# Kernel tuning notes

Measured on AMD Instinct MI355X. Metric: run time of the kernel, lower is better.

The kernel has to match this reference:

```python
import jax, jax.numpy as jnp
import numpy as np

IN_UNITS = 128
N_DRUG, N_DIS, N_EDGE = 10000, 5000, 2000000


def setup_inputs() -> dict:
    key = jax.random.key(0)
    ks = jax.random.split(key, 10)
    s1 = 1.0 / np.sqrt(2 * IN_UNITS)
    s2 = 1.0 / np.sqrt(128)
    s3 = 1.0 / np.sqrt(64)
    return {
        "drug_feat": jax.random.normal(ks[0], (N_DRUG, IN_UNITS), dtype=jnp.float32),
        "dis_feat": jax.random.normal(ks[1], (N_DIS, IN_UNITS), dtype=jnp.float32),
        "edge_index": jax.random.randint(ks[2], (2, N_EDGE), 0, N_DIS, dtype=jnp.int64),
        "W1": jax.random.uniform(ks[3], (128, 2 * IN_UNITS), jnp.float32, -s1, s1),
        "b1": jax.random.uniform(ks[4], (128,), jnp.float32, -s1, s1),
        "W2": jax.random.uniform(ks[5], (64, 128), jnp.float32, -s2, s2),
        "b2": jax.random.uniform(ks[6], (64,), jnp.float32, -s2, s2),
        "W3": jax.random.uniform(ks[7], (1, 64), jnp.float32, -s3, s3),
        "b3": jax.random.uniform(ks[8], (1,), jnp.float32, -s3, s3),
    }


def reference(drug_feat, dis_feat, edge_index, W1, b1, W2, b2, W3, b3):
    # Gather endpoint features and concat along feature dim: [E, 2*in_units]
    edge_feat = jnp.concatenate(
        (drug_feat[edge_index[0]], dis_feat[edge_index[1]]), axis=1
    )
    # 3-layer MLP (Dropout is identity in eval mode)
    h = jax.nn.relu(edge_feat @ W1.T + b1)  # [E, 128]
    h = jax.nn.relu(h @ W2.T + b2)          # [E, 64]
    return h @ W3.T + b3                     # [E, 1]
```

## Files before the change

kernel.cpp:

```cpp
#include <hip/hip_runtime.h>


typedef __bf16 bf16x8 __attribute__((ext_vector_type(8)));
typedef unsigned short u16x8 __attribute__((ext_vector_type(8)));
typedef float f32x4 __attribute__((ext_vector_type(4)));

static __device__ __forceinline__ unsigned short f2b(float f) {
  unsigned int u = __builtin_bit_cast(unsigned int, f);
  u += 0x7FFFu + ((u >> 16) & 1u);
  return (unsigned short)(u >> 16);
}

static __device__ __forceinline__ f32x4 mfma_bf16(u16x8 a, u16x8 b, f32x4 c) {
  return __builtin_amdgcn_mfma_f32_16x16x32_bf16(
      __builtin_bit_cast(bf16x8, a), __builtin_bit_cast(bf16x8, b), c, 0, 0, 0);
}

__global__ void cvt_tables(const float* __restrict__ a, const float* __restrict__ b,
                           unsigned short* __restrict__ oa, unsigned short* __restrict__ ob,
                           int na, int nb) {
  const int t = blockIdx.x * blockDim.x + threadIdx.x;
  const int ta = na >> 3;
  const float* src;
  unsigned short* dst;
  int i;
  if (t < ta) {
    src = a; dst = oa; i = t;
  } else {
    i = t - ta;
    if (i >= (nb >> 3)) return;
    src = b; dst = ob;
  }
  const float4 f0 = *(const float4*)(src + i * 8);
  const float4 f1 = *(const float4*)(src + i * 8 + 4);
  u16x8 v;
  v[0] = f2b(f0.x); v[1] = f2b(f0.y); v[2] = f2b(f0.z); v[3] = f2b(f0.w);
  v[4] = f2b(f1.x); v[5] = f2b(f1.y); v[6] = f2b(f1.z); v[7] = f2b(f1.w);
  *(u16x8*)(dst + i * 8) = v;
}

__global__ void cvt_weights(const float* __restrict__ W1, const float* __restrict__ W2,
                            unsigned short* __restrict__ o1, unsigned short* __restrict__ o2) {
  const int t = blockIdx.x * blockDim.x + threadIdx.x;
  if (t < 4096) {
    const int l = t & 63, kt = (t >> 6) & 7, nt = t >> 9;
    const int n = 16 * nt + (l & 15), k0 = 32 * kt + 8 * (l >> 4);
    const float* src = W1 + n * 256 + k0;
    u16x8 v;
#pragma unroll
    for (int j = 0; j < 8; ++j) v[j] = f2b(src[j]);
    *(u16x8*)(o1 + t * 8) = v;
  } else if (t < 5120) {
    const int u = t - 4096;
    const int l = u & 63, kt = (u >> 6) & 3, nt = u >> 8;
    const int n = 16 * nt + (l & 15), k0 = 32 * kt + 8 * (l >> 4);
    const float* src = W2 + n * 128 + k0;
    u16x8 v;
#pragma unroll
    for (int j = 0; j < 8; ++j) v[j] = f2b(src[j]);
    *(u16x8*)(o2 + u * 8) = v;
  }
}

__global__ __launch_bounds__(512, 4) void mlp_fused(
    const unsigned short* __restrict__ drugB, const unsigned short* __restrict__ disB,
    const int* __restrict__ eidx, const unsigned short* __restrict__ w1frag,
    const unsigned short* __restrict__ w2frag, const float* __restrict__ b1,
    const float* __restrict__ b2, const float* __restrict__ W3,
    const float* __restrict__ b3, float* __restrict__ out, int E) {
  __shared__ __align__(16) unsigned char smem[65536 + 2048];
  unsigned char* Abase = smem;
  float* partials = (float*)(smem + 65536);

  const int tid = threadIdx.x;
  const int w = tid >> 6;
  const int wm = w >> 2;
  const int wn = w & 3;
  const int l = tid & 63;
  const int l15 = l & 15;
  const int lq = l >> 4;
  const int e0 = blockIdx.x * 128;

  {
    const int r = tid >> 2;
    const int q = tid & 3;
    int e = e0 + r;
    if (e >= E) e = E - 1;
    const int idx = (q < 2) ? eidx[e] : eidx[E + e];
    const unsigned short* src = ((q < 2) ? drugB : disB) + (long)idx * 128 + (q & 1) * 64;
    unsigned char* rowp = Abase + r * 512;
    const int base = q * 128;
    const int swz = (r & 7) << 4;
#pragma unroll
    for (int c = 0; c < 8; ++c) {
      const u16x8 v = *(const u16x8*)(src + c * 8);
      *(u16x8*)(rowp + ((base + c * 16) ^ swz)) = v;
    }
  }

  u16x8 w2f[4];
#pragma unroll
  for (int kt = 0; kt < 4; ++kt)
    w2f[kt] = *(const u16x8*)(w2frag + ((wn * 4 + kt) * 64 + l) * 8);
  const float b1v0 = b1[32 * wn + l15];
  const float b1v1 = b1[32 * wn + 16 + l15];
  const float b2v = b2[16 * wn + l15];
  const float w3v = W3[16 * wn + l15];
  __syncthreads();

  f32x4 acc1[4][2];
#pragma unroll
  for (int mti = 0; mti < 4; ++mti) {
    acc1[mti][0] = (f32x4){0.f, 0.f, 0.f, 0.f};
    acc1[mti][1] = (f32x4){0.f, 0.f, 0.f, 0.f};
  }
  const unsigned short* w1p = w1frag + ((2 * wn) * 8 * 64 + l) * 8;
  u16x8 nf0 = *(const u16x8*)(w1p);
  u16x8 nf1 = *(const u16x8*)(w1p + 512 * 8);
#pragma unroll
  for (int kt = 0; kt < 8; ++kt) {
    const u16x8 c0 = nf0, c1 = nf1;
    if (kt < 7) {
      nf0 = *(const u16x8*)(w1p + (kt + 1) * 64 * 8);
      nf1 = *(const u16x8*)(w1p + (512 + (kt + 1) * 64) * 8);
    }
#pragma unroll
    for (int mti = 0; mti < 4; ++mti) {
      const int row = 16 * (4 * wm + mti) + l15;
      const u16x8 a = *(const u16x8*)(Abase + row * 512 + ((64 * kt + 16 * lq) ^ ((row & 7) << 4)));
      acc1[mti][0] = mfma_bf16(a, c0, acc1[mti][0]);
      acc1[mti][1] = mfma_bf16(a, c1, acc1[mti][1]);
    }
  }
  __syncthreads();

#pragma unroll
  for (int mti = 0; mti < 4; ++mti) {
#pragma unroll
    for (int ntl = 0; ntl < 2; ++ntl) {
      const int col = 32 * wn + 16 * ntl + l15;
      const float bv = ntl ? b1v1 : b1v0;
#pragma unroll
      for (int i = 0; i < 4; ++i) {
        const int row = 16 * (4 * wm + mti) + 4 * lq + i;
        float h = acc1[mti][ntl][i] + bv;
        h = h > 0.f ? h : 0.f;
        *(unsigned short*)(Abase + row * 256 + (((unsigned)col * 2) ^ ((row & 7) << 4))) = f2b(h);
      }
    }
  }
  __syncthreads();

  f32x4 acc2[4];
#pragma unroll
  for (int mti = 0; mti < 4; ++mti) acc2[mti] = (f32x4){0.f, 0.f, 0.f, 0.f};
#pragma unroll
  for (int kt = 0; kt < 4; ++kt) {
#pragma unroll
    for (int mti = 0; mti < 4; ++mti) {
      const int row = 16 * (4 * wm + mti) + l15;
      const u16x8 a = *(const u16x8*)(Abase + row * 256 + ((64 * kt + 16 * lq) ^ ((row & 7) << 4)));
      acc2[mti] = mfma_bf16(a, w2f[kt], acc2[mti]);
    }
  }

  float p[16];
#pragma unroll
  for (int mti = 0; mti < 4; ++mti)
#pragma unroll
    for (int i = 0; i < 4; ++i) {
      float h = acc2[mti][i] + b2v;
      h = h > 0.f ? h : 0.f;
      p[mti * 4 + i] = h * w3v;
    }
  float a8[8];
#pragma unroll
  for (int j = 0; j < 8; ++j) {
    const bool hi = (l15 & 1);
    const float give = hi ? p[2 * j] : p[2 * j + 1];
    const float keep = hi ? p[2 * j + 1] : p[2 * j];
    a8[j] = keep + __shfl_xor(give, 1, 64);
  }
  float a4[4];
#pragma unroll
  for (int j = 0; j < 4; ++j) {
    const bool hi = (l15 & 2);
    const float give = hi ? a8[2 * j] : a8[2 * j + 1];
    const float keep = hi ? a8[2 * j + 1] : a8[2 * j];
    a4[j] = keep + __shfl_xor(give, 2, 64);
  }
  float a2[2];
#pragma unroll
  for (int j = 0; j < 2; ++j) {
    const bool hi = (l15 & 4);
    const float give = hi ? a4[2 * j] : a4[2 * j + 1];
    const float keep = hi ? a4[2 * j + 1] : a4[2 * j];
    a2[j] = keep + __shfl_xor(give, 4, 64);
  }
  float d;
  {
    const bool hi = (l15 & 8);
    const float give = hi ? a2[0] : a2[1];
    const float keep = hi ? a2[1] : a2[0];
    d = keep + __shfl_xor(give, 8, 64);
  }
  const int row = 16 * (4 * wm + (l15 >> 2)) + 4 * lq + (l15 & 3);
  partials[wn * 128 + row] = d;
  __syncthreads();

  if (tid < 128) {
    const int e = e0 + tid;
    if (e < E) {
      out[e] = partials[tid] + partials[128 + tid] + partials[256 + tid] +
               partials[384 + tid] + b3[0];
    }
  }
}

extern "C" void kernel_launch(void* const* d_in, const int* in_sizes, int n_in,
                              void* d_out, int out_size, void* d_ws, size_t ws_size,
                              hipStream_t stream) {
  const float* drug = (const float*)d_in[0];
  const float* dis = (const float*)d_in[1];
  const int* eidx = (const int*)d_in[2];
  const float* W1 = (const float*)d_in[3];
  const float* b1 = (const float*)d_in[4];
  const float* W2 = (const float*)d_in[5];
  const float* b2 = (const float*)d_in[6];
  const float* W3 = (const float*)d_in[7];
  const float* b3 = (const float*)d_in[8];
  float* out = (float*)d_out;

  const int na = in_sizes[0];
  const int nb = in_sizes[1];
  const int E = in_sizes[2] / 2;

  unsigned short* ws = (unsigned short*)d_ws;
  unsigned short* drugB = ws;
  unsigned short* disB = ws + na;
  unsigned short* w1f = ws + na + nb;
  unsigned short* w2f = w1f + 128 * 256;

  const int tct = (na + nb) >> 3;
  cvt_tables<<<(tct + 255) / 256, 256, 0, stream>>>(drug, dis, drugB, disB, na, nb);
  cvt_weights<<<20, 256, 0, stream>>>(W1, W2, w1f, w2f);

  const int grid = (E + 127) / 128;
  mlp_fused<<<grid, 512, 0, stream>>>(drugB, disB, eidx, w1f, w2f, b1, b2, W3, b3, out, E);
}
```

Before: 273.8 us.

## Transpose MFMA operands so weights are A and edges are B, halve block size

Blocks now handle 64 edges with 256 threads (4 waves), and each wave owns a slice of output features across all 64 edges. The MFMA operands are swapped so weight fragments form the A operand and gathered edge rows form the B operand. This lets bias, ReLU and the W3 dot product run per lane over 4 consecutive features, replacing the long shuffle-reduction tree with two cross-lane xor shuffles, and lets layer-1 activations be stored as 8-byte ushort4 writes. Smaller blocks with half the shared memory should allow more resident blocks per CU, but each wave now reads more LDS A-tiles per weight fragment and there are twice as many blocks.

New measurement: 245.2 us. 10.4% less time.

```diff
diff --git a/kernel.cpp b/kernel.cpp
--- a/kernel.cpp
+++ b/kernel.cpp
@@ -43,8 +43,8 @@
                             unsigned short* __restrict__ o1, unsigned short* __restrict__ o2) {
   const int t = blockIdx.x * blockDim.x + threadIdx.x;
   if (t < 4096) {
-    const int l = t & 63, kt = (t >> 6) & 7, nt = t >> 9;
-    const int n = 16 * nt + (l & 15), k0 = 32 * kt + 8 * (l >> 4);
+    const int l = t & 63, kt = (t >> 6) & 7, ut = t >> 9;
+    const int n = 16 * ut + (l & 15), k0 = 32 * kt + 8 * (l >> 4);
     const float* src = W1 + n * 256 + k0;
     u16x8 v;
 #pragma unroll
@@ -62,24 +62,22 @@
   }
 }
 
-__global__ __launch_bounds__(512, 4) void mlp_fused(
+__global__ __launch_bounds__(256, 4) void mlp_fused(
     const unsigned short* __restrict__ drugB, const unsigned short* __restrict__ disB,
     const int* __restrict__ eidx, const unsigned short* __restrict__ w1frag,
     const unsigned short* __restrict__ w2frag, const float* __restrict__ b1,
     const float* __restrict__ b2, const float* __restrict__ W3,
     const float* __restrict__ b3, float* __restrict__ out, int E) {
-  __shared__ __align__(16) unsigned char smem[65536 + 2048];
+  __shared__ __align__(16) unsigned char smem[32768 + 1024];
   unsigned char* Abase = smem;
-  float* partials = (float*)(smem + 65536);
+  float* partials = (float*)(smem + 32768);
 
   const int tid = threadIdx.x;
-  const int w = tid >> 6;
-  const int wm = w >> 2;
-  const int wn = w & 3;
+  const int wn = tid >> 6;
   const int l = tid & 63;
   const int l15 = l & 15;
   const int lq = l >> 4;
-  const int e0 = blockIdx.x * 128;
+  const int e0 = blockIdx.x * 64;
 
   {
     const int r = tid >> 2;
@@ -102,19 +100,19 @@
 #pragma unroll
   for (int kt = 0; kt < 4; ++kt)
     w2f[kt] = *(const u16x8*)(w2frag + ((wn * 4 + kt) * 64 + l) * 8);
-  const float b1v0 = b1[32 * wn + l15];
-  const float b1v1 = b1[32 * wn + 16 + l15];
-  const float b2v = b2[16 * wn + l15];
-  const float w3v = W3[16 * wn + l15];
-  __syncthreads();
-
-  f32x4 acc1[4][2];
-#pragma unroll
-  for (int mti = 0; mti < 4; ++mti) {
-    acc1[mti][0] = (f32x4){0.f, 0.f, 0.f, 0.f};
-    acc1[mti][1] = (f32x4){0.f, 0.f, 0.f, 0.f};
-  }
-  const unsigned short* w1p = w1frag + ((2 * wn) * 8 * 64 + l) * 8;
+  const float4 b1v0 = *(const float4*)(b1 + 32 * wn + 4 * lq);
+  const float4 b1v1 = *(const float4*)(b1 + 32 * wn + 16 + 4 * lq);
+  const float4 b2v = *(const float4*)(b2 + 16 * wn + 4 * lq);
+  const float4 w3v = *(const float4*)(W3 + 16 * wn + 4 * lq);
+  __syncthreads();
+
+  f32x4 acc1[2][4];
+#pragma unroll
+  for (int uti = 0; uti < 2; ++uti)
+#pragma unroll
+    for (int nt = 0; nt < 4; ++nt) acc1[uti][nt] = (f32x4){0.f, 0.f, 0.f, 0.f};
+
+  const unsigned short* w1p = w1frag + ((2 * wn) * 512 + l) * 8;
   u16x8 nf0 = *(const u16x8*)(w1p);
   u16x8 nf1 = *(const u16x8*)(w1p + 512 * 8);
 #pragma unroll
@@ -125,94 +123,63 @@
       nf1 = *(const u16x8*)(w1p + (512 + (kt + 1) * 64) * 8);
     }
 #pragma unroll
-    for (int mti = 0; mti < 4; ++mti) {
-      const int row = 16 * (4 * wm + mti) + l15;
-      const u16x8 a = *(const u16x8*)(Abase + row * 512 + ((64 * kt + 16 * lq) ^ ((row & 7) << 4)));
-      acc1[mti][0] = mfma_bf16(a, c0, acc1[mti][0]);
-      acc1[mti][1] = mfma_bf16(a, c1, acc1[mti][1]);
-    }
-  }
-  __syncthreads();
-
-#pragma unroll
-  for (int mti = 0; mti < 4; ++mti) {
-#pragma unroll
-    for (int ntl = 0; ntl < 2; ++ntl) {
-      const int col = 32 * wn + 16 * ntl + l15;
-      const float bv = ntl ? b1v1 : b1v0;
-#pragma unroll
-      for (int i = 0; i < 4; ++i) {
-        const int row = 16 * (4 * wm + mti) + 4 * lq + i;
-        float h = acc1[mti][ntl][i] + bv;
-        h = h > 0.f ? h : 0.f;
-        *(unsigned short*)(Abase + row * 256 + (((unsigned)col * 2) ^ ((row & 7) << 4))) = f2b(h);
-      }
+    for (int nt = 0; nt < 4; ++nt) {
+      const int e = 16 * nt + l15;
+      const u16x8 b = *(const u16x8*)(Abase + e * 512 + ((64 * kt + 16 * lq) ^ ((e & 7) << 4)));
+      acc1[0][nt] = mfma_bf16(c0, b, acc1[0][nt]);
+      acc1[1][nt] = mfma_bf16(c1, b, acc1[1][nt]);
+    }
+  }
+  __syncthreads();
+
+#pragma unroll
+  for (int uti = 0; uti < 2; ++uti) {
+    const float4 bv = uti ? b1v1 : b1v0;
+#pragma unroll
+    for (int nt = 0; nt < 4; ++nt) {
+      const int e = 16 * nt + l15;
+      float h0 = acc1[uti][nt][0] + bv.x; h0 = h0 > 0.f ? h0 : 0.f;
+      float h1 = acc1[uti][nt][1] + bv.y; h1 = h1 > 0.f ? h1 : 0.f;
+      float h2 = acc1[uti][nt][2] + bv.z; h2 = h2 > 0.f ? h2 : 0.f;
+      float h3 = acc1[uti][nt][3] + bv.w; h3 = h3 > 0.f ? h3 : 0.f;
+      ushort4 hv;
+      hv.x = f2b(h0); hv.y = f2b(h1); hv.z = f2b(h2); hv.w = f2b(h3);
+      *(ushort4*)(Abase + e * 256 + ((64 * wn + 32 * uti + 8 * lq) ^ ((e & 7) << 4))) = hv;
     }
   }
   __syncthreads();
 
   f32x4 acc2[4];
 #pragma unroll
-  for (int mti = 0; mti < 4; ++mti) acc2[mti] = (f32x4){0.f, 0.f, 0.f, 0.f};
+  for (int nt = 0; nt < 4; ++nt) acc2[nt] = (f32x4){0.f, 0.f, 0.f, 0.f};
 #pragma unroll
   for (int kt = 0; kt < 4; ++kt) {
 #pragma unroll
-    for (int mti = 0; mti < 4; ++mti) {
-      const int row = 16 * (4 * wm + mti) + l15;
-      const u16x8 a = *(const u16x8*)(Abase + row * 256 + ((64 * kt + 16 * lq) ^ ((row & 7) << 4)));
-      acc2[mti] = mfma_bf16(a, w2f[kt], acc2[mti]);
-    }
-  }
-
-  float p[16];
-#pragma unroll
-  for (int mti = 0; mti < 4; ++mti)
-#pragma unroll
-    for (int i = 0; i < 4; ++i) {
-      float h = acc2[mti][i] + b2v;
-      h = h > 0.f ? h : 0.f;
-      p[mti * 4 + i] = h * w3v;
-    }
-  float a8[8];
-#pragma unroll
-  for (int j = 0; j < 8; ++j) {
-    const bool hi = (l15 & 1);
-    const float give = hi ? p[2 * j] : p[2 * j + 1];
-    const float keep = hi ? p[2 * j + 1] : p[2 * j];
-    a8[j] = keep + __shfl_xor(give, 1, 64);
-  }
-  float a4[4];
-#pragma unroll
-  for (int j = 0; j < 4; ++j) {
-    const bool hi = (l15 & 2);
-    const float give = hi ? a8[2 * j] : a8[2 * j + 1];
-    const float keep = hi ? a8[2 * j + 1] : a8[2 * j];
-    a4[j] = keep + __shfl_xor(give, 2, 64);
-  }
-  float a2[2];
-#pragma unroll
-  for (int j = 0; j < 2; ++j) {
-    const bool hi = (l15 & 4);
-    const float give = hi ? a4[2 * j] : a4[2 * j + 1];
-    const float keep = hi ? a4[2 * j + 1] : a4[2 * j];
-    a2[j] = keep + __shfl_xor(give, 4, 64);
-  }
-  float d;
-  {
-    const bool hi = (l15 & 8);
-    const float give = hi ? a2[0] : a2[1];
-    const float keep = hi ? a2[1] : a2[0];
-    d = keep + __shfl_xor(give, 8, 64);
-  }
-  const int row = 16 * (4 * wm + (l15 >> 2)) + 4 * lq + (l15 & 3);
-  partials[wn * 128 + row] = d;
-  __syncthreads();
-
-  if (tid < 128) {
+    for (int nt = 0; nt < 4; ++nt) {
+      const int e = 16 * nt + l15;
+      const u16x8 b = *(const u16x8*)(Abase + e * 256 + ((64 * kt + 16 * lq) ^ ((e & 7) << 4)));
+      acc2[nt] = mfma_bf16(w2f[kt], b, acc2[nt]);
+    }
+  }
+
+#pragma unroll
+  for (int nt = 0; nt < 4; ++nt) {
+    float h0 = acc2[nt][0] + b2v.x; h0 = h0 > 0.f ? h0 : 0.f;
+    float h1 = acc2[nt][1] + b2v.y; h1 = h1 > 0.f ? h1 : 0.f;
+    float h2 = acc2[nt][2] + b2v.z; h2 = h2 > 0.f ? h2 : 0.f;
+    float h3 = acc2[nt][3] + b2v.w; h3 = h3 > 0.f ? h3 : 0.f;
+    float s = h0 * w3v.x + h1 * w3v.y + h2 * w3v.z + h3 * w3v.w;
+    s += __shfl_xor(s, 16, 64);
+    s += __shfl_xor(s, 32, 64);
+    if (l < 16) partials[wn * 64 + 16 * nt + l15] = s;
+  }
+  __syncthreads();
+
+  if (tid < 64) {
     const int e = e0 + tid;
     if (e < E) {
-      out[e] = partials[tid] + partials[128 + tid] + partials[256 + tid] +
-               partials[384 + tid] + b3[0];
+      out[e] = partials[tid] + partials[64 + tid] + partials[128 + tid] +
+               partials[192 + tid] + b3[0];
     }
   }
 }
@@ -245,6 +212,6 @@
   cvt_tables<<<(tct + 255) / 256, 256, 0, stream>>>(drug, dis, drugB, disB, na, nb);
   cvt_weights<<<20, 256, 0, stream>>>(W1, W2, w1f, w2f);
 
-  const int grid = (E + 127) / 128;
-  mlp_fused<<<grid, 512, 0, stream>>>(drugB, disB, eidx, w1f, w2f, b1, b2, W3, b3, out, E);
-}
+  const int grid = (E + 63) / 64;
+  mlp_fused<<<grid, 256, 0, stream>>>(drugB, disB, eidx, w1f, w2f, b1, b2, W3, b3, out, E);
+}
```
